# Performance work log

Measured on AMD Instinct MI355X. Metric: run time of the kernel, lower is better.

## Reference

```python
import jax, jax.numpy as jnp
import numpy as np

N_WIRES = 10
N_OPS = 30
C64 = jnp.complex64

# Frozen random circuit (stand-in for tq.RandomLayer(n_ops=30)): deterministic op list.
_rng = np.random.default_rng(42)
OPS = []
for _ in range(N_OPS):
    k = int(_rng.integers(0, 4))
    if k == 3:
        w = _rng.choice(N_WIRES, size=2, replace=False)
        OPS.append(('cnot', int(w[0]), int(w[1])))
    else:
        OPS.append((('rx', 'ry', 'rz')[k], int(_rng.integers(0, N_WIRES)), -1))


def _rx_mat(t):
    c = jnp.cos(t / 2).astype(C64)
    s = jnp.sin(t / 2).astype(C64)
    return jnp.stack([jnp.stack([c, -1j * s]), jnp.stack([-1j * s, c])])


def _ry_mat(t):
    c = jnp.cos(t / 2).astype(C64)
    s = jnp.sin(t / 2).astype(C64)
    return jnp.stack([jnp.stack([c, -s]), jnp.stack([s, c])])


def _rz_mat(t):
    tc = t.astype(C64)
    z = jnp.zeros((), C64)
    return jnp.stack([jnp.stack([jnp.exp(-1j * tc / 2), z]), jnp.stack([z, jnp.exp(1j * tc / 2)])])

_GATE = {'rx': _rx_mat, 'ry': _ry_mat, 'rz': _rz_mat}


def _apply_1q(state, U, w):
    # state: [bsz] + [2]*N_WIRES ; apply 2x2 U on qubit axis w
    s = jnp.moveaxis(state, 1 + w, -1)
    s = jnp.einsum('ij,...j->...i', U, s)
    return jnp.moveaxis(s, -1, 1 + w)


def _apply_cnot(state, c, t):
    s = jnp.moveaxis(state, (1 + c, 1 + t), (-2, -1))
    s = jnp.stack([s[..., 0, :], s[..., 1, ::-1]], axis=-2)  # flip target when control=1
    return jnp.moveaxis(s, (-2, -1), (1 + c, 1 + t))


def _quantum_head(x, rand_params, rx_theta, ry_theta, head_w, head_b):
    bsz = x.shape[0]
    # GeneralEncoder '10xRy': RY(x[:,w])|0> per wire -> product state built directly
    state = jnp.ones((bsz, 1), C64)
    for w in range(N_WIRES):
        vec = jnp.stack([jnp.cos(x[:, w] / 2), jnp.sin(x[:, w] / 2)], axis=-1).astype(C64)
        state = (state[:, :, None] * vec[:, None, :]).reshape(bsz, -1)
    state = state.reshape((bsz,) + (2,) * N_WIRES)
    # RandomLayer (frozen 30-op circuit, one angle per op)
    for i, (kind, a, b) in enumerate(OPS):
        if kind == 'cnot':
            state = _apply_cnot(state, a, b)
        else:
            state = _apply_1q(state, _GATE[kind](rand_params[i]), a)
    # shared trainable RX then RY applied to every wire (single shared param each)
    Urx = _rx_mat(rx_theta[0])
    Ury = _ry_mat(ry_theta[0])
    for w in range(N_WIRES):
        state = _apply_1q(state, Urx, w)
        state = _apply_1q(state, Ury, w)
    # MeasureAll(PauliZ): <Z_w> = P(bit_w=0) - P(bit_w=1)
    probs = jnp.abs(state) ** 2  # float32, [bsz] + [2]*n
    feats = []
    for w in range(N_WIRES):
        axes = tuple(1 + q for q in range(N_WIRES) if q != w)
        p = probs.sum(axis=axes)  # [bsz, 2]
        feats.append(p[:, 0] - p[:, 1])
    feats = jnp.stack(feats, axis=-1)  # [bsz, n_wires]
    return feats @ head_w + head_b[0]


def _mlp(x, w0, b0, w1, b1, w2, b2, w3, b3):
    # faithful to ClassicalMLP: Linear chain with NO activations
    h = x @ w0.T + b0
    h = h @ w1.T + b1
    h = h @ w2.T + b2
    return (h @ w3.T + b3)[:, 0]


def setup_inputs() -> dict:
    key = jax.random.key(0)
    ks = jax.random.split(key, 14)
    BSZ = 8192
    return {
        'state_batch': jax.random.normal(ks[0], (BSZ, N_WIRES), jnp.float32),
        'rand_params': jax.random.normal(ks[1], (N_OPS,), jnp.float32),
        'rx_theta': jax.random.normal(ks[2], (1,), jnp.float32),
        'ry_theta': jax.random.normal(ks[3], (1,), jnp.float32),
        'head_w': jax.random.normal(ks[4], (N_WIRES,), jnp.float32) * 0.3,
        'head_b': jax.random.normal(ks[5], (1,), jnp.float32) * 0.1,
        'w0': jax.random.normal(ks[6], (64, N_WIRES), jnp.float32) * 0.3,
        'b0': jax.random.normal(ks[7], (64,), jnp.float32) * 0.1,
        'w1': jax.random.normal(ks[8], (32, 64), jnp.float32) * 0.12,
        'b1': jax.random.normal(ks[9], (32,), jnp.float32) * 0.1,
        'w2': jax.random.normal(ks[10], (16, 32), jnp.float32) * 0.17,
        'b2': jax.random.normal(ks[11], (16,), jnp.float32) * 0.1,
        'w3': jax.random.normal(ks[12], (1, 16), jnp.float32) * 0.25,
        'b3': jax.random.normal(ks[13], (1,), jnp.float32) * 0.1,
    }


def reference(state_batch, rand_params, rx_theta, ry_theta, head_w, head_b, w0, b0, w1, b1, w2, b2, w3, b3):
    q = _quantum_head(state_batch, rand_params, rx_theta, ry_theta, head_w, head_b)
    c = _mlp(state_batch, w0, b0, w1, b1, w2, b2, w3, b3)
    return q + c
```

## Files before the change

kernel.cpp:

```cpp
#include <hip/hip_runtime.h>
#include <cstdint>

#define NW 10
#define NOPS 30

namespace {

typedef unsigned __int128 u128;

struct CRng { u128 state; u128 inc; bool has32; uint32_t cached; };

constexpr u128 PCG_MUL = (((u128)0x2360ED051FC65DA4ULL) << 64) | (u128)0x4385DF649FCCF645ULL;

constexpr void cr_step(CRng &r) { r.state = r.state * PCG_MUL + r.inc; }

constexpr uint64_t cr_out(u128 st) {
  uint64_t hi = (uint64_t)(st >> 64);
  uint64_t lo = (uint64_t)st;
  unsigned rot = (unsigned)(st >> 122) & 63u;
  uint64_t v = hi ^ lo;
  return (v >> rot) | (v << ((64u - rot) & 63u));
}

constexpr uint64_t cr_next64(CRng &r) { cr_step(r); return cr_out(r.state); }

constexpr uint32_t cr_next32(CRng &r) {
  if (r.has32) { r.has32 = false; return r.cached; }
  uint64_t v = cr_next64(r);
  r.has32 = true; r.cached = (uint32_t)(v >> 32);
  return (uint32_t)v;
}

constexpr CRng cr_seed(uint32_t ent) {
  uint32_t pool[4] = {0u, 0u, 0u, 0u};
  uint32_t hc = 0x43b0d7e5u;
  for (int i = 0; i < 4; i++) {
    uint32_t v = (i == 0) ? ent : 0u;
    v ^= hc; hc *= 0x931e8875u; v *= hc; v ^= v >> 16;
    pool[i] = v;
  }
  for (int s = 0; s < 4; s++)
    for (int d = 0; d < 4; d++)
      if (s != d) {
        uint32_t v = pool[s];
        v ^= hc; hc *= 0x931e8875u; v *= hc; v ^= v >> 16;
        uint32_t res = 0xca01f9ddu * pool[d] - 0x4973f715u * v;
        res ^= res >> 16;
        pool[d] = res;
      }
  uint32_t hb = 0x8b51f9ddu;
  uint64_t s64[4] = {0ull, 0ull, 0ull, 0ull};
  for (int i = 0; i < 8; i++) {
    uint32_t d = pool[i & 3];
    d ^= hb; hb *= 0x58f38dedu; d *= hb; d ^= d >> 16;
    if (i & 1) s64[i >> 1] |= ((uint64_t)d << 32); else s64[i >> 1] = (uint64_t)d;
  }
  CRng r{};
  u128 initstate = (((u128)s64[0]) << 64) | (u128)s64[1];
  u128 initseq   = (((u128)s64[2]) << 64) | (u128)s64[3];
  r.state = 0; r.inc = (initseq << 1) | (u128)1;
  cr_step(r);
  r.state += initstate;
  cr_step(r);
  r.has32 = false; r.cached = 0u;
  return r;
}

constexpr uint32_t cr_lemire32(CRng &r, uint32_t rng) {
  uint32_t rng_excl = rng + 1u;
  uint64_t m = (uint64_t)cr_next32(r) * (uint64_t)rng_excl;
  uint32_t leftover = (uint32_t)m;
  if (leftover < rng_excl) {
    uint32_t threshold = (uint32_t)(0xFFFFFFFFu - rng) % rng_excl;
    while (leftover < threshold) {
      m = (uint64_t)cr_next32(r) * (uint64_t)rng_excl;
      leftover = (uint32_t)m;
    }
  }
  return (uint32_t)(m >> 32);
}

constexpr bool canary_pcg42() {
  CRng r = cr_seed(42u);
  double a = (double)(cr_next64(r) >> 11) * (1.0 / 9007199254740992.0);
  double b = (double)(cr_next64(r) >> 11) * (1.0 / 9007199254740992.0);
  double c = (double)(cr_next64(r) >> 11) * (1.0 / 9007199254740992.0);
  bool ok = (a > 0.77395603) && (a < 0.77395607);
  ok = ok && (b > 0.43887842) && (b < 0.43887846);
  ok = ok && (c > 0.85859790) && (c < 0.85859794);
  return ok;
}
static_assert(canary_pcg42(), "CANARY_PCG_SEED42_RANDOM_MISMATCH");

struct COp { int kind; int a; int b; int slot; };
struct Circ { COp op[NOPS]; };

constexpr Circ build_circuit() {
  Circ c{};
  CRng r = cr_seed(42u);
  for (int i = 0; i < NOPS; i++) {
    int k = (int)cr_lemire32(r, 3u);
    if (k == 3) {
      uint32_t v8 = cr_lemire32(r, 8u);
      uint32_t v9 = cr_lemire32(r, 9u);
      uint32_t i0 = v8;
      uint32_t i1 = (v9 == v8) ? 9u : v9;
      uint32_t j = cr_lemire32(r, 1u);
      if (j == 0u) { uint32_t t = i0; i0 = i1; i1 = t; }
      c.op[i] = COp{3, (int)i0, (int)i1, i};
    } else {
      int w = (int)cr_lemire32(r, 9u);
      c.op[i] = COp{k, w, 0, i};
    }
  }
  return c;
}
constexpr Circ CC = build_circuit();

constexpr int MAXP = 16384;
constexpr int MAXU = 4096;

struct Tables {
  int np, nu, overflow;
  uint32_t pmeta[MAXP]; uint32_t pcm[MAXP]; uint32_t psm[MAXP];
  uint32_t ukey[MAXU];  int ustart[MAXU + 1];
  uint32_t upk[MAXU];
};

constexpr Tables build_tables() {
  Tables T{};
  uint32_t meta[MAXP] = {}; uint32_t cm[MAXP] = {}; uint32_t sm[MAXP] = {};
  int np = 0; int ovf = 0;
  for (int w = 0; w < NW; w++)
    for (int src = 0; src < 3; src++) {
      uint32_t xm = (src != 0) ? (1u << w) : 0u;
      uint32_t zm = (src != 1) ? (1u << w) : 0u;
      meta[np] = xm | (zm << 10) | ((uint32_t)w << 21) | ((uint32_t)src << 25);
      cm[np] = 0u; sm[np] = 0u; np++;
    }
  for (int k = NOPS - 1; k >= 0 && !ovf; k--) {
    const COp op = CC.op[k];
    if (op.kind == 3) {
      const int c = op.a, t = op.b;
      for (int p = 0; p < np; p++) {
        uint32_t m = meta[p];
        uint32_t xm = m & 1023u, zm = (m >> 10) & 1023u;
        uint32_t xc = (xm >> c) & 1u, zc = (zm >> c) & 1u;
        uint32_t xt = (xm >> t) & 1u, zt = (zm >> t) & 1u;
        uint32_t fl = xc & zt & (1u ^ (xt ^ zc));
        xm ^= xc << t;
        zm ^= zt << c;
        m = (m & ~(1023u | (1023u << 10))) | xm | (zm << 10);
        m ^= fl << 20;
        meta[p] = m;
      }
    } else {
      const int q = op.a, ax = op.kind, bit = op.slot;
      const int n0 = np;
      for (int p = 0; p < n0; p++) {
        uint32_t m = meta[p];
        uint32_t x = (m >> q) & 1u;
        uint32_t z = (m >> (10 + q)) & 1u;
        uint32_t viol = (ax == 0) ? z : (ax == 1) ? (x ^ z) : x;
        if (viol) {
          uint32_t nx = 0, nz = 0, fl = 0;
          if (ax == 0)      { if (x) { nx = 0; nz = 1; fl = 1; } else { nx = 1; nz = 1; fl = 0; } }
          else if (ax == 1) { if (x) { nx = 0; nz = 1; fl = 0; } else { nx = 1; nz = 0; fl = 1; } }
          else              { if (z) { nx = 1; nz = 0; fl = 0; } else { nx = 1; nz = 1; fl = 1; } }
          if (np >= MAXP) { ovf = 1; break; }
          uint32_t m2 = m;
          m2 &= ~((1u << q) | (1u << (10 + q)));
          m2 |= (nx << q) | (nz << (10 + q));
          m2 ^= fl << 20;
          meta[np] = m2; cm[np] = cm[p]; sm[np] = sm[p] | (1u << bit);
          np++;
          cm[p] |= 1u << bit;
        }
      }
    }
  }
  if (ovf) { T.overflow = 1; return T; }
  int n2 = 0;
  for (int p = 0; p < np; p++) {
    uint32_t m = meta[p];
    if ((m & 1023u) & ((m >> 10) & 1023u)) continue;
    meta[n2] = m; cm[n2] = cm[p]; sm[n2] = sm[p]; n2++;
  }
  np = n2;
  int idx[MAXP] = {}; int tmp[MAXP] = {};
  for (int i = 0; i < np; i++) idx[i] = i;
  int hist[1025] = {};
  for (int i = 0; i < 1025; i++) hist[i] = 0;
  for (int i = 0; i < np; i++) hist[1 + (meta[idx[i]] & 1023u)]++;
  for (int i = 0; i < 1024; i++) hist[i + 1] += hist[i];
  for (int i = 0; i < np; i++) tmp[hist[meta[idx[i]] & 1023u]++] = idx[i];
  for (int i = 0; i < 1025; i++) hist[i] = 0;
  for (int i = 0; i < np; i++) hist[1 + ((meta[tmp[i]] >> 10) & 1023u)]++;
  for (int i = 0; i < 1024; i++) hist[i + 1] += hist[i];
  for (int i = 0; i < np; i++) idx[hist[(meta[tmp[i]] >> 10) & 1023u]++] = tmp[i];
  int nu = 0; uint32_t prev = 0xFFFFFFFFu;
  for (int i = 0; i < np; i++) {
    int p = idx[i];
    uint32_t key = meta[p] & 0xFFFFFu;
    if (key != prev) {
      if (nu >= MAXU) { T.overflow = 2; return T; }
      T.ukey[nu] = key; T.ustart[nu] = i; prev = key; nu++;
    }
    T.pmeta[i] = meta[p]; T.pcm[i] = cm[p]; T.psm[i] = sm[p];
  }
  T.ustart[nu] = np;
  for (int u = 0; u < nu; u++) {
    uint32_t key = T.ukey[u]; uint32_t pk = 0;
    for (int p = 0; p < 5; p++) {
      uint32_t x2 = (key >> (2 * p)) & 3u;
      uint32_t z2 = (key >> (10 + 2 * p)) & 3u;
      pk |= ((x2 | (z2 << 2)) << 2) << (6 * p);
    }
    T.upk[u] = pk;
  }
  T.np = np; T.nu = nu; T.overflow = 0;
  return T;
}

constexpr Tables TT = build_tables();
static_assert(TT.overflow == 0, "PAULI_PATH_OVERFLOW_raise_MAXP_or_pivot_to_runtime_tables");
static_assert(TT.nu >= 1 && TT.nu <= MAXU, "PAULI_UNIQUE_COUNT_OUT_OF_RANGE");
constexpr int NU  = TT.nu;
constexpr int NUP = (NU + 1) & ~1;

}

__device__ const Tables dTT = TT;

#define BLOCK 1024
#define WPB   16

__global__ __launch_bounds__(BLOCK) void fused_kernel(
    const float* __restrict__ x,
    const float* __restrict__ rand_params,
    const float* __restrict__ rx_theta, const float* __restrict__ ry_theta,
    const float* __restrict__ head_w, const float* __restrict__ head_b,
    const float* __restrict__ w0, const float* __restrict__ b0,
    const float* __restrict__ w1, const float* __restrict__ b1,
    const float* __restrict__ w2, const float* __restrict__ b2,
    const float* __restrict__ w3, const float* __restrict__ b3,
    float* __restrict__ out, int bsz)
{
  __shared__ __align__(16) float2 CKsh[NUP];
  __shared__ float Tbl[WPB][80];
  __shared__ float ct[32], st[32], abr[3], hwsh[10];
  __shared__ float r2[32], r1[64];
  __shared__ float MLPsh[NW + 1];

  const int tid  = threadIdx.x;
  const int wave = tid >> 6;
  const int lane = tid & 63;

  if (tid < NOPS) {
    float t = rand_params[tid];
    ct[tid] = cosf(t);
    st[tid] = sinf(t);
  } else if (tid == 32) {
    float tx = rx_theta[0], ty = ry_theta[0];
    abr[0] = cosf(tx) * cosf(ty);
    abr[1] = -sinf(ty);
    abr[2] = sinf(tx) * cosf(ty);
  } else if (tid >= 64 && tid < 96) {
    const int j = tid - 64;
    float acc = 0.f;
    for (int k = 0; k < 16; k++) acc += w3[k] * w2[k * 32 + j];
    r2[j] = acc;
  } else if (tid >= 96 && tid < 96 + NW) {
    hwsh[tid - 96] = head_w[tid - 96];
  }
  __syncthreads();

  for (int u = tid; u < NU; u += BLOCK) {
    float acc = 0.f;
    const int i0 = dTT.ustart[u], i1 = dTT.ustart[u + 1];
    for (int i = i0; i < i1; i++) {
      uint32_t m = dTT.pmeta[i];
      float v = hwsh[(m >> 21) & 15u] * abr[(m >> 25) & 3u];
      if (m & (1u << 20)) v = -v;
      uint32_t c = dTT.pcm[i];
      while (c) { int b = __builtin_ctz(c); v *= ct[b]; c &= c - 1u; }
      uint32_t s = dTT.psm[i];
      while (s) { int b = __builtin_ctz(s); v *= st[b]; s &= s - 1u; }
      acc += v;
    }
    CKsh[u] = make_float2(acc, __uint_as_float(dTT.upk[u]));
  }
  if (NU < NUP && tid == 0) CKsh[NU] = make_float2(0.f, __uint_as_float(0u));
  if (tid >= BLOCK - 64) {
    const int j = tid - (BLOCK - 64);
    float acc = 0.f;
    for (int k = 0; k < 32; k++) acc += r2[k] * w1[k * 64 + j];
    r1[j] = acc;
  }
  __syncthreads();

  if (tid < NW) {
    float acc = 0.f;
    for (int k = 0; k < 64; k++) acc += r1[k] * w0[k * NW + tid];
    MLPsh[tid] = acc;
  } else if (tid == NW) {
    float acc = b3[0] + head_b[0];
    for (int k = 0; k < 16; k++) acc += w3[k] * b2[k];
    for (int k = 0; k < 32; k++) acc += r2[k] * b1[k];
    for (int k = 0; k < 64; k++) acc += r1[k] * b0[k];
    MLPsh[NW] = acc;
  }

  const int wv = blockIdx.x * WPB + wave;
  const bool live = (wv < bsz);
  const float* xe = x + wv * NW;
  float* tbl = Tbl[wave];
  if (live) {
    {
      const int e = lane;
      const int p = e >> 4, code = e & 15;
      float2 xv = *(const float2*)(xe + 2 * p);
      float c0 = __cosf(xv.x), s0 = __sinf(xv.x);
      float c1 = __cosf(xv.y), s1 = __sinf(xv.y);
      float f0 = (code & 1) ? s0 : ((code & 4) ? c0 : 1.0f);
      float f1 = (code & 2) ? s1 : ((code & 8) ? c1 : 1.0f);
      tbl[e] = f0 * f1;
    }
    if (lane < 16) {
      const int e = lane + 64;
      const int p = e >> 4, code = e & 15;
      float2 xv = *(const float2*)(xe + 2 * p);
      float c0 = __cosf(xv.x), s0 = __sinf(xv.x);
      float c1 = __cosf(xv.y), s1 = __sinf(xv.y);
      float f0 = (code & 1) ? s0 : ((code & 4) ? c0 : 1.0f);
      float f1 = (code & 2) ? s1 : ((code & 8) ? c1 : 1.0f);
      tbl[e] = f0 * f1;
    }
  }
  __syncthreads();
  if (!live) return;

  const char* tb = (const char*)tbl;
  float acc0 = 0.f, acc1 = 0.f;
#pragma unroll 4
  for (int s = 2 * lane; s < NUP; s += 128) {
    float4 q = *(const float4*)&CKsh[s];
    uint32_t ka = __float_as_uint(q.y);
    uint32_t kb = __float_as_uint(q.w);
    float a0 = *(const float*)(tb +       ( ka        & 63u));
    float a1 = *(const float*)(tb +  64 + ((ka >>  6) & 63u));
    float a2 = *(const float*)(tb + 128 + ((ka >> 12) & 63u));
    float a3 = *(const float*)(tb + 192 + ((ka >> 18) & 63u));
    float a4 = *(const float*)(tb + 256 + ((ka >> 24) & 63u));
    float b0v = *(const float*)(tb +       ( kb        & 63u));
    float b1v = *(const float*)(tb +  64 + ((kb >>  6) & 63u));
    float b2v = *(const float*)(tb + 128 + ((kb >> 12) & 63u));
    float b3v = *(const float*)(tb + 192 + ((kb >> 18) & 63u));
    float b4v = *(const float*)(tb + 256 + ((kb >> 24) & 63u));
    acc0 = fmaf(q.x, ((a0 * a1) * (a2 * a3)) * a4, acc0);
    acc1 = fmaf(q.z, ((b0v * b1v) * (b2v * b3v)) * b4v, acc1);
  }
  float acc = acc0 + acc1;

#pragma unroll
  for (int m = 1; m < 64; m <<= 1) acc += __shfl_xor(acc, m);

  if (lane == 0) {
    float cc = MLPsh[NW];
#pragma unroll
    for (int w = 0; w < NW; w++) cc += xe[w] * MLPsh[w];
    out[wv] = acc + cc;
  }
}

extern "C" void kernel_launch(void* const* d_in, const int* in_sizes, int n_in,
                              void* d_out, int out_size, void* d_ws, size_t ws_size,
                              hipStream_t stream) {
  const float* x   = (const float*)d_in[0];
  const float* rp  = (const float*)d_in[1];
  const float* rxT = (const float*)d_in[2];
  const float* ryT = (const float*)d_in[3];
  const float* hw  = (const float*)d_in[4];
  const float* hb  = (const float*)d_in[5];
  const float* w0  = (const float*)d_in[6];
  const float* b0  = (const float*)d_in[7];
  const float* w1  = (const float*)d_in[8];
  const float* b1  = (const float*)d_in[9];
  const float* w2  = (const float*)d_in[10];
  const float* b2  = (const float*)d_in[11];
  const float* w3  = (const float*)d_in[12];
  const float* b3  = (const float*)d_in[13];
  const int bsz = in_sizes[0] / NW;

  const int blocks = (bsz + WPB - 1) / WPB;
  hipLaunchKernelGGL(fused_kernel, dim3(blocks), dim3(BLOCK), 0, stream,
                     x, rp, rxT, ryT, hw, hb, w0, b0, w1, b1, w2, b2, w3, b3,
                     (float*)d_out, bsz);
}
```

Baseline: 100.4 us.

## Flatten Pauli-path coefficient reduction with base-3 trig product tables and LDS atomics

Replaces the per-unique-key serial loop over Pauli paths, which walks cos/sin bitmasks with ctz loops, with a flat parallel loop over all paths. Each path looks up six precomputed products of cos/sin over 5-op groups, encoded as base-3 digits in packed words, and the results are accumulated into shared memory with atomicAdd. Paths are permuted by a stride coprime to the path count so that concurrent atomics spread across different unique keys. The per-wave x-table build is moved before the first barrier so it overlaps the setup work. The trade-off is an extra 6x243 shared table, a larger constant table, and LDS atomic contention.

```diff
diff --git a/kernel.cpp b/kernel.cpp
--- a/kernel.cpp
+++ b/kernel.cpp
@@ -125,6 +125,7 @@
   uint32_t pmeta[MAXP]; uint32_t pcm[MAXP]; uint32_t psm[MAXP];
   uint32_t ukey[MAXU];  int ustart[MAXU + 1];
   uint32_t upk[MAXU];
+  uint32_t pa[MAXP]; uint32_t pb[MAXP]; uint16_t pu[MAXP];
 };
 
 constexpr Tables build_tables() {
@@ -198,6 +199,7 @@
   for (int i = 0; i < np; i++) hist[1 + ((meta[tmp[i]] >> 10) & 1023u)]++;
   for (int i = 0; i < 1024; i++) hist[i + 1] += hist[i];
   for (int i = 0; i < np; i++) idx[hist[(meta[tmp[i]] >> 10) & 1023u]++] = tmp[i];
+  uint16_t puTmp[MAXP] = {};
   int nu = 0; uint32_t prev = 0xFFFFFFFFu;
   for (int i = 0; i < np; i++) {
     int p = idx[i];
@@ -207,6 +209,7 @@
       T.ukey[nu] = key; T.ustart[nu] = i; prev = key; nu++;
     }
     T.pmeta[i] = meta[p]; T.pcm[i] = cm[p]; T.psm[i] = sm[p];
+    puTmp[i] = (uint16_t)(nu - 1);
   }
   T.ustart[nu] = np;
   for (int u = 0; u < nu; u++) {
@@ -218,6 +221,29 @@
     }
     T.upk[u] = pk;
   }
+  int P = 997;
+  {
+    bool ok = false;
+    while (!ok) {
+      int a = P, b = np;
+      while (b) { int t2 = a % b; a = b; b = t2; }
+      if (a == 1) ok = true; else P++;
+    }
+  }
+  constexpr int POW3[5] = {1, 3, 9, 27, 81};
+  for (int j = 0; j < np; j++) {
+    int i = (int)(((long long)j * P) % np);
+    uint32_t cmv = T.pcm[i], smv = T.psm[i], m = T.pmeta[i];
+    uint32_t g[6] = {0, 0, 0, 0, 0, 0};
+    uint32_t mm = cmv;
+    while (mm) { int b = __builtin_ctz(mm); mm &= mm - 1u; g[b / 5] += (uint32_t)POW3[b % 5]; }
+    mm = smv;
+    while (mm) { int b = __builtin_ctz(mm); mm &= mm - 1u; g[b / 5] += 2u * (uint32_t)POW3[b % 5]; }
+    T.pa[j] = g[0] | (g[1] << 8) | (g[2] << 16) | (g[3] << 24);
+    T.pb[j] = g[4] | (g[5] << 8) | (((m >> 21) & 15u) << 16)
+            | (((m >> 25) & 3u) << 20) | (((m >> 20) & 1u) << 22);
+    T.pu[j] = puTmp[i];
+  }
   T.np = np; T.nu = nu; T.overflow = 0;
   return T;
 }
@@ -227,6 +253,7 @@
 static_assert(TT.nu >= 1 && TT.nu <= MAXU, "PAULI_UNIQUE_COUNT_OUT_OF_RANGE");
 constexpr int NU  = TT.nu;
 constexpr int NUP = (NU + 1) & ~1;
+constexpr int NP  = TT.np;
 
 }
 
@@ -234,6 +261,7 @@
 
 #define BLOCK 1024
 #define WPB   16
+#define PWRK  (BLOCK - 16)
 
 __global__ __launch_bounds__(BLOCK) void fused_kernel(
     const float* __restrict__ x,
@@ -247,6 +275,7 @@
     float* __restrict__ out, int bsz)
 {
   __shared__ __align__(16) float2 CKsh[NUP];
+  __shared__ float Gt[6 * 243];
   __shared__ float Tbl[WPB][80];
   __shared__ float ct[32], st[32], abr[3], hwsh[10];
   __shared__ float r2[32], r1[64];
@@ -255,6 +284,11 @@
   const int tid  = threadIdx.x;
   const int wave = tid >> 6;
   const int lane = tid & 63;
+
+  const int wv = blockIdx.x * WPB + wave;
+  const bool live = (wv < bsz);
+  const float* xe = x + wv * NW;
+  float* tbl = Tbl[wave];
 
   if (tid < NOPS) {
     float t = rand_params[tid];
@@ -265,32 +299,52 @@
     abr[0] = cosf(tx) * cosf(ty);
     abr[1] = -sinf(ty);
     abr[2] = sinf(tx) * cosf(ty);
+  } else if (tid >= 40 && tid < 40 + NW) {
+    hwsh[tid - 40] = head_w[tid - 40];
   } else if (tid >= 64 && tid < 96) {
     const int j = tid - 64;
     float acc = 0.f;
     for (int k = 0; k < 16; k++) acc += w3[k] * w2[k * 32 + j];
     r2[j] = acc;
-  } else if (tid >= 96 && tid < 96 + NW) {
-    hwsh[tid - 96] = head_w[tid - 96];
+  }
+  for (int i = tid; i < NUP; i += BLOCK)
+    CKsh[i] = make_float2(0.f, __uint_as_float(i < NU ? dTT.upk[i] : 0u));
+  if (live) {
+    {
+      const int e = lane;
+      const int p = e >> 4, code = e & 15;
+      float2 xv = *(const float2*)(xe + 2 * p);
+      float c0 = __cosf(xv.x), s0 = __sinf(xv.x);
+      float c1 = __cosf(xv.y), s1 = __sinf(xv.y);
+      float f0 = (code & 1) ? s0 : ((code & 4) ? c0 : 1.0f);
+      float f1 = (code & 2) ? s1 : ((code & 8) ? c1 : 1.0f);
+      tbl[e] = f0 * f1;
+    }
+    if (lane < 16) {
+      const int e = lane + 64;
+      const int p = e >> 4, code = e & 15;
+      float2 xv = *(const float2*)(xe + 2 * p);
+      float c0 = __cosf(xv.x), s0 = __sinf(xv.x);
+      float c1 = __cosf(xv.y), s1 = __sinf(xv.y);
+      float f0 = (code & 1) ? s0 : ((code & 4) ? c0 : 1.0f);
+      float f1 = (code & 2) ? s1 : ((code & 8) ? c1 : 1.0f);
+      tbl[e] = f0 * f1;
+    }
   }
   __syncthreads();
 
-  for (int u = tid; u < NU; u += BLOCK) {
-    float acc = 0.f;
-    const int i0 = dTT.ustart[u], i1 = dTT.ustart[u + 1];
-    for (int i = i0; i < i1; i++) {
-      uint32_t m = dTT.pmeta[i];
-      float v = hwsh[(m >> 21) & 15u] * abr[(m >> 25) & 3u];
-      if (m & (1u << 20)) v = -v;
-      uint32_t c = dTT.pcm[i];
-      while (c) { int b = __builtin_ctz(c); v *= ct[b]; c &= c - 1u; }
-      uint32_t s = dTT.psm[i];
-      while (s) { int b = __builtin_ctz(s); v *= st[b]; s &= s - 1u; }
-      acc += v;
-    }
-    CKsh[u] = make_float2(acc, __uint_as_float(dTT.upk[u]));
-  }
-  if (NU < NUP && tid == 0) CKsh[NU] = make_float2(0.f, __uint_as_float(0u));
+  for (int e = tid; e < 6 * 243; e += BLOCK) {
+    const int g = e / 243;
+    int c = e - g * 243;
+    float v = 1.f;
+#pragma unroll
+    for (int j = 0; j < 5; j++) {
+      int tr = c % 3; c /= 3;
+      if (tr == 1) v *= ct[5 * g + j];
+      else if (tr == 2) v *= st[5 * g + j];
+    }
+    Gt[e] = v;
+  }
   if (tid >= BLOCK - 64) {
     const int j = tid - (BLOCK - 64);
     float acc = 0.f;
@@ -309,32 +363,17 @@
     for (int k = 0; k < 32; k++) acc += r2[k] * b1[k];
     for (int k = 0; k < 64; k++) acc += r1[k] * b0[k];
     MLPsh[NW] = acc;
-  }
-
-  const int wv = blockIdx.x * WPB + wave;
-  const bool live = (wv < bsz);
-  const float* xe = x + wv * NW;
-  float* tbl = Tbl[wave];
-  if (live) {
-    {
-      const int e = lane;
-      const int p = e >> 4, code = e & 15;
-      float2 xv = *(const float2*)(xe + 2 * p);
-      float c0 = __cosf(xv.x), s0 = __sinf(xv.x);
-      float c1 = __cosf(xv.y), s1 = __sinf(xv.y);
-      float f0 = (code & 1) ? s0 : ((code & 4) ? c0 : 1.0f);
-      float f1 = (code & 2) ? s1 : ((code & 8) ? c1 : 1.0f);
-      tbl[e] = f0 * f1;
-    }
-    if (lane < 16) {
-      const int e = lane + 64;
-      const int p = e >> 4, code = e & 15;
-      float2 xv = *(const float2*)(xe + 2 * p);
-      float c0 = __cosf(xv.x), s0 = __sinf(xv.x);
-      float c1 = __cosf(xv.y), s1 = __sinf(xv.y);
-      float f0 = (code & 1) ? s0 : ((code & 4) ? c0 : 1.0f);
-      float f1 = (code & 2) ? s1 : ((code & 8) ? c1 : 1.0f);
-      tbl[e] = f0 * f1;
+  } else if (tid >= 16) {
+    for (int i = tid - 16; i < NP; i += PWRK) {
+      uint32_t pa = dTT.pa[i];
+      uint32_t pb = dTT.pb[i];
+      int      u  = (int)dTT.pu[i];
+      float v = hwsh[(pb >> 16) & 15u] * abr[(pb >> 20) & 3u];
+      if (pb & (1u << 22)) v = -v;
+      v *= Gt[         (pa       ) & 255u] * Gt[1 * 243 + ((pa >>  8) & 255u)];
+      v *= Gt[2 * 243 + ((pa >> 16) & 255u)] * Gt[3 * 243 + ( pa >> 24        )];
+      v *= Gt[4 * 243 + ( pb        & 255u)] * Gt[5 * 243 + ((pb >>  8) & 255u)];
+      atomicAdd(&CKsh[u].x, v);
     }
   }
   __syncthreads();
```

New measurement: 91.51 us. -8.9%, faster.
